# Performance work log

Measured on AMD Instinct MI355X. Metric: run time of the kernel, lower is better.

The kernel has to match this reference:

```python
import jax, jax.numpy as jnp
import numpy as np

N_HEADS = 16
DIM = 1024
HEAD_DIM = DIM // N_HEADS

def setup_inputs() -> dict:
    key = jax.random.key(0)
    ks = jax.random.split(key, 5)
    x = jax.random.normal(ks[0], (4, 2048, DIM), dtype=jnp.float32)
    W_attn = jax.random.normal(ks[1], (DIM, 3 * DIM), dtype=jnp.float32) / np.sqrt(DIM)
    b_attn = jnp.zeros((3 * DIM,), dtype=jnp.float32)
    W_proj = jax.random.normal(ks[2], (DIM, DIM), dtype=jnp.float32) / np.sqrt(DIM)
    b_proj = jnp.zeros((DIM,), dtype=jnp.float32)
    return {"x": x, "W_attn": W_attn, "b_attn": b_attn, "W_proj": W_proj, "b_proj": b_proj}

def reference(x, W_attn, b_attn, W_proj, b_proj):
    B, S, D = x.shape
    qkv = x @ W_attn + b_attn                      # [B,S,3D]
    q, k, v = jnp.split(qkv, 3, axis=2)
    def heads(t):
        return t.reshape(B, S, N_HEADS, HEAD_DIM).transpose(0, 2, 1, 3)  # [B,H,S,hd]
    qh, kh, vh = heads(q), heads(k), heads(v)
    scale = 1.0 / np.sqrt(HEAD_DIM).astype(np.float32)
    scores = jnp.einsum('bhqd,bhkd->bhqk', qh, kh) * scale  # [B,H,S,S]
    causal = jnp.tril(jnp.ones((S, S), dtype=bool))
    scores = jnp.where(causal, scores, -jnp.inf)
    probs = jax.nn.softmax(scores, axis=-1)
    ctx = jnp.einsum('bhqk,bhkd->bhqd', probs, vh)           # [B,H,S,hd]
    ctx = ctx.transpose(0, 2, 1, 3).reshape(B, S, D)
    return ctx @ W_proj + b_proj
```

## Files before the change

kernel.cpp:

```cpp
#include <hip/hip_runtime.h>
#include <hip/hip_bf16.h>
#include <stdint.h>

typedef __attribute__((ext_vector_type(4))) float  f32x4a;
typedef __attribute__((ext_vector_type(8))) short  bf16x8s;
typedef __attribute__((ext_vector_type(8))) unsigned short u16x8;

#define QSCALE 0.18033688011112042f

static __device__ __forceinline__ unsigned short f2bf(float f) {
    union { float f; uint32_t u; } v; v.f = f;
    uint32_t u = v.u;
    return (unsigned short)((u + 0x7FFFu + ((u >> 16) & 1u)) >> 16);
}

static __device__ __forceinline__ unsigned int pack2bf(float lo, float hi) {
    __hip_bfloat162 t = __float22bfloat162_rn(make_float2(lo, hi));
    union { __hip_bfloat162 b; unsigned int u; } c; c.b = t;
    return c.u;
}

static __device__ __forceinline__ float exp2a(float x) {
    float r;
    asm("v_exp_f32 %0, %1" : "=v"(r) : "v"(x));
    return r;
}

#define GLL(src, dst)                                                          \
    __builtin_amdgcn_global_load_lds(                                          \
        (const __attribute__((address_space(1))) void*)(src),                  \
        (__attribute__((address_space(3))) void*)(dst), 16, 0, 0)

__global__ __launch_bounds__(256) void k_cvt_bf16(const float* __restrict__ in,
                                                  unsigned short* __restrict__ out, int n8) {
    int i = blockIdx.x * blockDim.x + threadIdx.x;
    if (i >= n8) return;
    const float4* p = (const float4*)(in + (size_t)i * 8);
    float4 a = p[0], b = p[1];
    u16x8 o;
    o[0] = f2bf(a.x); o[1] = f2bf(a.y); o[2] = f2bf(a.z); o[3] = f2bf(a.w);
    o[4] = f2bf(b.x); o[5] = f2bf(b.y); o[6] = f2bf(b.z); o[7] = f2bf(b.w);
    *(u16x8*)(out + (size_t)i * 8) = o;
}

__global__ __launch_bounds__(256) void k_scale_bias(const float* __restrict__ b,
                                                    float* __restrict__ out,
                                                    int n, int nscale, float sc) {
    int i = blockIdx.x * blockDim.x + threadIdx.x;
    if (i >= n) return;
    out[i] = b[i] * (i < nscale ? sc : 1.0f);
}

__global__ __launch_bounds__(256) void k_transpose_w(const float* __restrict__ W,
                                                     unsigned short* __restrict__ Wt,
                                                     int K, int N, float sc, int nscale) {
    __shared__ float tile[64][68];
    int bx = blockIdx.x;
    int ntn = N >> 6;
    int kt = bx / ntn, nt = bx % ntn;
    int t = threadIdx.x;
    int r0 = t >> 4;
    int c4 = (t & 15) << 2;
    for (int i = 0; i < 4; ++i) {
        int k = r0 + i * 16;
        float4 v = *(const float4*)(W + (size_t)(kt * 64 + k) * N + nt * 64 + c4);
        tile[k][c4 + 0] = v.x; tile[k][c4 + 1] = v.y;
        tile[k][c4 + 2] = v.z; tile[k][c4 + 3] = v.w;
    }
    __syncthreads();
    int nl = t >> 2;
    int kc = (t & 3) << 4;
    float s = (nt * 64 + nl < nscale) ? sc : 1.0f;
    unsigned short* dst = Wt + (size_t)(nt * 64 + nl) * K + kt * 64 + kc;
    u16x8 o0, o1;
    for (int i = 0; i < 8; ++i) o0[i] = f2bf(tile[kc + i][nl] * s);
    for (int i = 0; i < 8; ++i) o1[i] = f2bf(tile[kc + 8 + i][nl] * s);
    *(u16x8*)dst = o0;
    *(u16x8*)(dst + 8) = o1;
}

template<int OUT_BF16, int VW>
__global__ __launch_bounds__(512, 4) void k_gemm2b(const unsigned short* __restrict__ A,
                                                   const unsigned short* __restrict__ Bt,
                                                   const float* __restrict__ bias,
                                                   void* __restrict__ Cout,
                                                   unsigned short* __restrict__ vt,
                                                   int M, int N, int K, int ntn) {
    __shared__ __align__(16) unsigned short S[3][12288];
    unsigned short* Sf = &S[0][0];

    int nwg = gridDim.x;
    int bid = blockIdx.x;
    int wg = (bid & 7) * (nwg >> 3) + (bid >> 3);
    int mt = wg / ntn, nt = wg % ntn;
    size_t m0 = (size_t)mt * 128, n0 = (size_t)nt * 256;

    int tid = threadIdx.x;
    int w = tid >> 6, lane = tid & 63;
    int wm = w >> 2, wn = w & 3;
    int l15 = lane & 15, l4 = lane >> 4;

    int srow = tid >> 2;
    int sch = (tid & 3) ^ ((srow >> 1) & 3);
    const unsigned short* Asrc = A  + (m0 + srow) * (size_t)K + sch * 8;
    const unsigned short* Bsrc = Bt + (n0 + srow) * (size_t)K + sch * 8;

#define STG(bufoff, kt)                                                                   \
    do {                                                                                  \
        GLL(Asrc + (size_t)(kt) * 32,                    Sf + (bufoff) + tid * 8);        \
        GLL(Bsrc + (size_t)(kt) * 32,                    Sf + (bufoff) + 4096 + tid * 8); \
        GLL(Bsrc + (size_t)(kt) * 32 + (size_t)128 * K,  Sf + (bufoff) + 8192 + tid * 8); \
    } while (0)

    int ck = (l4 ^ ((l15 >> 1) & 3)) * 8;
    int aoff = (wm * 64 + l15) * 32 + ck;
    int boff = 4096 + (wn * 64 + l15) * 32 + ck;

    f32x4a acc[4][4] = {};

#define BAR() __builtin_amdgcn_s_barrier()

    int NT = K >> 5;

    STG(0, 0);
    STG(12288, 1);
    asm volatile("s_waitcnt vmcnt(3)" ::: "memory");
    __builtin_amdgcn_sched_barrier(0);
    BAR();

    int cb = 0;
    for (int t = 0; t < NT; ++t) {
        int sb = cb + 24576; if (sb >= 36864) sb -= 36864;
        bool more = (t + 2) < NT;
        if (more) STG(sb, t + 2);
        bf16x8s af[4], bf[4];
        #pragma unroll
        for (int q = 0; q < 4; ++q) af[q] = *(const bf16x8s*)(Sf + cb + aoff + q * 512);
        #pragma unroll
        for (int q = 0; q < 4; ++q) bf[q] = *(const bf16x8s*)(Sf + cb + boff + q * 512);
        __builtin_amdgcn_s_setprio(1);
        #pragma unroll
        for (int mf = 0; mf < 4; ++mf)
            #pragma unroll
            for (int nf = 0; nf < 4; ++nf)
                acc[mf][nf] = __builtin_amdgcn_mfma_f32_16x16x32_bf16(af[mf], bf[nf],
                                                                      acc[mf][nf], 0, 0, 0);
        __builtin_amdgcn_s_setprio(0);
        if (more) { asm volatile("s_waitcnt vmcnt(3)" ::: "memory"); }
        else      { asm volatile("s_waitcnt vmcnt(0)" ::: "memory"); }
        __builtin_amdgcn_sched_barrier(0);
        BAR();
        cb += 12288; if (cb >= 36864) cb = 0;
    }

    if (VW && nt >= 8) {
        int b = (int)(m0 >> 11);
        int sb_ = ((int)m0 & 2047) + wm * 64;
        #pragma unroll
        for (int nf = 0; nf < 4; ++nf) {
            int vc = ((int)n0 - 2048) + wn * 64 + nf * 16 + l15;
            int h = vc >> 6, d = vc & 63;
            float bv = bias[2048 + vc];
            unsigned short* vrow = vt + ((size_t)(b * 16 + h) * 64 + d) * 2048;
            #pragma unroll
            for (int mf = 0; mf < 4; ++mf) {
                int s = sb_ + mf * 16 + l4 * 4;
                uint2 pv = make_uint2(pack2bf(acc[mf][nf][0] + bv, acc[mf][nf][1] + bv),
                                      pack2bf(acc[mf][nf][2] + bv, acc[mf][nf][3] + bv));
                *(uint2*)(vrow + s) = pv;
            }
        }
    } else {
        #pragma unroll
        for (int nf = 0; nf < 4; ++nf) {
            int col = (int)n0 + wn * 64 + nf * 16 + l15;
            float bv = bias[col];
            #pragma unroll
            for (int mf = 0; mf < 4; ++mf) {
                int rbase = (int)m0 + wm * 64 + mf * 16 + l4 * 4;
                #pragma unroll
                for (int rr = 0; rr < 4; ++rr) {
                    float v = acc[mf][nf][rr] + bv;
                    if (OUT_BF16)
                        ((unsigned short*)Cout)[(size_t)(rbase + rr) * N + col] = f2bf(v);
                    else
                        ((float*)Cout)[(size_t)(rbase + rr) * N + col] = v;
                }
            }
        }
    }
#undef STG
#undef BAR
}

__global__ __launch_bounds__(256, 4) void k_attn(const unsigned short* __restrict__ qkv,
                                                 const unsigned short* __restrict__ vt,
                                                 unsigned short* __restrict__ ctx) {
    __shared__ unsigned short Ks[2][4096];
    __shared__ unsigned short Vs[2][4096];
    __shared__ unsigned short Pb[4][1024];
    int bx = blockIdx.x;
    int bh = bx & 63;
    int pr = bx >> 6;
    int b = bh >> 4, hd = bh & 15;
    int tid = threadIdx.x;
    int w = tid >> 6, lane = tid & 63;
    int l15 = lane & 15, l4 = lane >> 4;

    const unsigned short* Qb  = qkv + (size_t)b * 2048 * 3072 + hd * 64;
    const unsigned short* Kb  = Qb + 1024;
    const unsigned short* Vtb = vt + (size_t)bh * 64 * 2048;

    int kr0 = tid >> 3, kc0 = tid & 7;
    int kr1 = (tid + 256) >> 3, kc1 = tid & 7;
    const unsigned short* Ksr0 = Kb  + (size_t)kr0 * 3072 + ((kc0 ^ (kr0 & 7)) << 3);
    const unsigned short* Ksr1 = Kb  + (size_t)kr1 * 3072 + ((kc1 ^ (kr1 & 7)) << 3);
    const unsigned short* Vsr0 = Vtb + (size_t)kr0 * 2048 + ((kc0 ^ (kr0 & 7)) << 3);
    const unsigned short* Vsr1 = Vtb + (size_t)kr1 * 2048 + ((kc1 ^ (kr1 & 7)) << 3);
    unsigned short* pbw = &Pb[w][0];

    int prow = l15 * 64;
    int psw  = l15 & 7;
    int ph   = (l4 & 1) * 4;
    int pc0  = ((0 + (l4 >> 1)) ^ psw) * 8;
    int pc1  = ((2 + (l4 >> 1)) ^ psw) * 8;
    int pc2  = ((4 + (l4 >> 1)) ^ psw) * 8;
    int pc3  = ((6 + (l4 >> 1)) ^ psw) * 8;
    int pr0  = ((0 + l4) ^ psw) * 8;
    int pr1  = ((4 + l4) ^ psw) * 8;

#define STAGE(buf, kv0s)                                                                        \
    do {                                                                                        \
        size_t ko_ = (size_t)(kv0s) * 3072;                                                     \
        GLL(Ksr0 + ko_,     &Ks[buf][w * 512]);                                                 \
        GLL(Ksr1 + ko_,     &Ks[buf][2048 + w * 512]);                                          \
        GLL(Vsr0 + (kv0s),  &Vs[buf][w * 512]);                                                 \
        GLL(Vsr1 + (kv0s),  &Vs[buf][2048 + w * 512]);                                          \
    } while (0)

    for (int half = 0; half < 2; ++half) {
        int j = half ? (31 - pr) : pr;
        int q0 = j * 64 + w * 16;
        int qa = q0 + l15;
        bf16x8s qf0, qf1;
        {
            const unsigned short* p = Qb + (size_t)(q0 + l15) * 3072 + l4 * 8;
            qf0 = *(const bf16x8s*)p;
            qf1 = *(const bf16x8s*)(p + 32);
        }
        f32x4a o[4] = {};
        float lrow = 0.0f;
        const int NSTEPS = j + 1;

        STAGE(0, 0);
        __syncthreads();

        int s = 0;
        while (true) {
            int cur = s & 1;
            int kv0 = s << 6;
            if (s + 1 < NSTEPS) STAGE(cur ^ 1, kv0 + 64);

            const unsigned short* Kbuf = Ks[cur];
            const unsigned short* Vbuf = Vs[cur];

            f32x4a z[4];
            __builtin_amdgcn_s_setprio(1);
            #pragma unroll
            for (int f = 0; f < 4; ++f) {
                int rk = f * 16 + l15;
                bf16x8s ka = *(const bf16x8s*)(Kbuf + rk * 64 + ((l4 ^ psw) << 3));
                bf16x8s kb = *(const bf16x8s*)(Kbuf + rk * 64 + (((4 + l4) ^ psw) << 3));
                f32x4a zz = {0.f, 0.f, 0.f, 0.f};
                zz = __builtin_amdgcn_mfma_f32_16x16x32_bf16(ka, qf0, zz, 0, 0, 0);
                zz = __builtin_amdgcn_mfma_f32_16x16x32_bf16(kb, qf1, zz, 0, 0, 0);
                z[f] = zz;
            }
            __builtin_amdgcn_s_setprio(0);

            bf16x8s vf[2][4];
            #pragma unroll
            for (int g = 0; g < 2; ++g)
                #pragma unroll
                for (int nf = 0; nf < 4; ++nf) {
                    int rv = nf * 16 + l15;
                    vf[g][nf] = *(const bf16x8s*)(Vbuf + rv * 64 + (((g * 4 + l4) ^ (rv & 7)) << 3));
                }

            if (s == NSTEPS - 1) {
                #pragma unroll
                for (int f = 0; f < 4; ++f)
                    #pragma unroll
                    for (int r = 0; r < 4; ++r)
                        if (kv0 + f * 16 + l4 * 4 + r > qa) z[f][r] = -1e30f;
            }

            f32x4a p4[4];
            #pragma unroll
            for (int f = 0; f < 4; ++f)
                #pragma unroll
                for (int r = 0; r < 4; ++r)
                    p4[f][r] = exp2a(z[f][r]);

            f32x4a ps = (p4[0] + p4[1]) + (p4[2] + p4[3]);
            float psum = (ps[0] + ps[1]) + (ps[2] + ps[3]);
            psum += __shfl_xor(psum, 16);
            psum += __shfl_xor(psum, 32);
            lrow += psum;

            unsigned int pk[8];
            #pragma unroll
            for (int f = 0; f < 4; ++f) {
                pk[2 * f]     = pack2bf(p4[f][0], p4[f][1]);
                pk[2 * f + 1] = pack2bf(p4[f][2], p4[f][3]);
            }

            *(uint2*)(pbw + prow + pc0 + ph) = make_uint2(pk[0], pk[1]);
            *(uint2*)(pbw + prow + pc1 + ph) = make_uint2(pk[2], pk[3]);
            *(uint2*)(pbw + prow + pc2 + ph) = make_uint2(pk[4], pk[5]);
            *(uint2*)(pbw + prow + pc3 + ph) = make_uint2(pk[6], pk[7]);
            asm volatile("" ::: "memory");
            bf16x8s pa0 = *(const bf16x8s*)(pbw + prow + pr0);
            bf16x8s pa1 = *(const bf16x8s*)(pbw + prow + pr1);
            asm volatile("" ::: "memory");

            __builtin_amdgcn_s_setprio(1);
            #pragma unroll
            for (int nf = 0; nf < 4; ++nf)
                o[nf] = __builtin_amdgcn_mfma_f32_16x16x32_bf16(pa0, vf[0][nf], o[nf], 0, 0, 0);
            #pragma unroll
            for (int nf = 0; nf < 4; ++nf)
                o[nf] = __builtin_amdgcn_mfma_f32_16x16x32_bf16(pa1, vf[1][nf], o[nf], 0, 0, 0);
            __builtin_amdgcn_s_setprio(0);

            ++s;
            if (s == NSTEPS) break;
            __syncthreads();
        }
        __syncthreads();

        float linv[4];
        #pragma unroll
        for (int r = 0; r < 4; ++r) linv[r] = 1.0f / __shfl(lrow, l4 * 4 + r);
        #pragma unroll
        for (int nf = 0; nf < 4; ++nf) {
            int col = hd * 64 + nf * 16 + l15;
            #pragma unroll
            for (int r = 0; r < 4; ++r) {
                int row = q0 + l4 * 4 + r;
                ctx[((size_t)b * 2048 + row) * 1024 + col] = f2bf(o[nf][r] * linv[r]);
            }
        }
    }
#undef STAGE
}

extern "C" void kernel_launch(void* const* d_in, const int* in_sizes, int n_in,
                              void* d_out, int out_size, void* d_ws, size_t ws_size,
                              hipStream_t stream) {
    const float* x      = (const float*)d_in[0];
    const float* W_attn = (const float*)d_in[1];
    const float* b_attn = (const float*)d_in[2];
    const float* W_proj = (const float*)d_in[3];
    const float* b_proj = (const float*)d_in[4];

    char* ws = (char*)d_ws;
    unsigned short* xb  = (unsigned short*)ws; ws += (size_t)8192 * 1024 * 2;
    unsigned short* wta = (unsigned short*)ws; ws += (size_t)3072 * 1024 * 2;
    unsigned short* wtp = (unsigned short*)ws; ws += (size_t)1024 * 1024 * 2;
    unsigned short* qkv = (unsigned short*)ws; ws += (size_t)8192 * 3072 * 2;
    unsigned short* vt  = (unsigned short*)ws; ws += (size_t)64 * 64 * 2048 * 2;
    unsigned short* ctx = (unsigned short*)ws; ws += (size_t)8192 * 1024 * 2;
    float*          sbias = (float*)ws;

    k_cvt_bf16<<<4096, 256, 0, stream>>>(x, xb, 8192 * 1024 / 8);
    k_transpose_w<<<16 * 48, 256, 0, stream>>>(W_attn, wta, 1024, 3072, QSCALE, 1024);
    k_transpose_w<<<16 * 16, 256, 0, stream>>>(W_proj, wtp, 1024, 1024, 1.0f, 0);
    k_scale_bias<<<12, 256, 0, stream>>>(b_attn, sbias, 3072, 1024, QSCALE);
    k_gemm2b<1, 1><<<768, 512, 0, stream>>>(xb, wta, sbias, (void*)qkv, vt, 8192, 3072, 1024, 12);
    k_attn<<<1024, 256, 0, stream>>>(qkv, vt, ctx);
    k_gemm2b<0, 0><<<256, 512, 0, stream>>>(ctx, wtp, b_proj, d_out, nullptr, 8192, 1024, 1024, 4);
}
```

Baseline: 161.9 us.

## Enlarge attention query tile to 128 rows so each K/V tile serves two query groups

Result: no change. 160.8 us (-0.6%).

```diff
diff --git a/kernel.cpp b/kernel.cpp
--- a/kernel.cpp
+++ b/kernel.cpp
@@ -193,12 +193,12 @@
 #undef BAR
 }
 
-__global__ __launch_bounds__(256, 4) void k_attn(const unsigned short* __restrict__ qkv,
+__global__ __launch_bounds__(256, 2) void k_attn(const unsigned short* __restrict__ qkv,
                                                  const unsigned short* __restrict__ vt,
                                                  unsigned short* __restrict__ ctx) {
     __shared__ unsigned short Ks[2][4096];
     __shared__ unsigned short Vs[2][4096];
-    __shared__ unsigned short Pb[4][1024];
+    __shared__ unsigned short Pb[4][2048];
     int bx = blockIdx.x;
     int bh = bx & 63;
     int pr = bx >> 6;
@@ -219,7 +219,6 @@
     const unsigned short* Vsr1 = Vtb + (size_t)kr1 * 2048 + ((kc1 ^ (kr1 & 7)) << 3);
     unsigned short* pbw = &Pb[w][0];
 
-    int prow = l15 * 64;
     int psw  = l15 & 7;
     int ph   = (l4 & 1) * 4;
     int pc0  = ((0 + (l4 >> 1)) ^ psw) * 8;
@@ -228,6 +227,8 @@
     int pc3  = ((6 + (l4 >> 1)) ^ psw) * 8;
     int pr0  = ((0 + l4) ^ psw) * 8;
     int pr1  = ((4 + l4) ^ psw) * 8;
+    int prow0 = l15 * 64;
+    int prow1 = (l15 + 16) * 64;
 
 #define STAGE(buf, kv0s)                                                                        \
     do {                                                                                        \
@@ -239,18 +240,21 @@
     } while (0)
 
     for (int half = 0; half < 2; ++half) {
-        int j = half ? (31 - pr) : pr;
-        int q0 = j * 64 + w * 16;
-        int qa = q0 + l15;
-        bf16x8s qf0, qf1;
+        int j = half ? (15 - pr) : pr;
+        int q0 = j * 128 + w * 32;
+        int qa0 = q0 + l15, qa1 = q0 + 16 + l15;
+        bf16x8s qf[2][2];
         {
-            const unsigned short* p = Qb + (size_t)(q0 + l15) * 3072 + l4 * 8;
-            qf0 = *(const bf16x8s*)p;
-            qf1 = *(const bf16x8s*)(p + 32);
-        }
-        f32x4a o[4] = {};
-        float lrow = 0.0f;
-        const int NSTEPS = j + 1;
+            const unsigned short* p0 = Qb + (size_t)(q0 + l15) * 3072 + l4 * 8;
+            qf[0][0] = *(const bf16x8s*)p0;
+            qf[0][1] = *(const bf16x8s*)(p0 + 32);
+            const unsigned short* p1 = p0 + (size_t)16 * 3072;
+            qf[1][0] = *(const bf16x8s*)p1;
+            qf[1][1] = *(const bf16x8s*)(p1 + 32);
+        }
+        f32x4a o[2][4] = {};
+        float lrow0 = 0.0f, lrow1 = 0.0f;
+        const int NSTEPS = 2 * j + 2;
 
         STAGE(0, 0);
         __syncthreads();
@@ -261,77 +265,103 @@
             int kv0 = s << 6;
             if (s + 1 < NSTEPS) STAGE(cur ^ 1, kv0 + 64);
 
-            const unsigned short* Kbuf = Ks[cur];
-            const unsigned short* Vbuf = Vs[cur];
-
-            f32x4a z[4];
-            __builtin_amdgcn_s_setprio(1);
-            #pragma unroll
-            for (int f = 0; f < 4; ++f) {
-                int rk = f * 16 + l15;
-                bf16x8s ka = *(const bf16x8s*)(Kbuf + rk * 64 + ((l4 ^ psw) << 3));
-                bf16x8s kb = *(const bf16x8s*)(Kbuf + rk * 64 + (((4 + l4) ^ psw) << 3));
-                f32x4a zz = {0.f, 0.f, 0.f, 0.f};
-                zz = __builtin_amdgcn_mfma_f32_16x16x32_bf16(ka, qf0, zz, 0, 0, 0);
-                zz = __builtin_amdgcn_mfma_f32_16x16x32_bf16(kb, qf1, zz, 0, 0, 0);
-                z[f] = zz;
+            if (kv0 <= q0 + 31) {
+                const unsigned short* Kbuf = Ks[cur];
+                const unsigned short* Vbuf = Vs[cur];
+
+                f32x4a z[2][4];
+                __builtin_amdgcn_s_setprio(1);
+                #pragma unroll
+                for (int f = 0; f < 4; ++f) {
+                    int rk = f * 16 + l15;
+                    bf16x8s ka = *(const bf16x8s*)(Kbuf + rk * 64 + ((l4 ^ psw) << 3));
+                    bf16x8s kb = *(const bf16x8s*)(Kbuf + rk * 64 + (((4 + l4) ^ psw) << 3));
+                    #pragma unroll
+                    for (int g = 0; g < 2; ++g) {
+                        f32x4a zz = {0.f, 0.f, 0.f, 0.f};
+                        zz = __builtin_amdgcn_mfma_f32_16x16x32_bf16(ka, qf[g][0], zz, 0, 0, 0);
+                        zz = __builtin_amdgcn_mfma_f32_16x16x32_bf16(kb, qf[g][1], zz, 0, 0, 0);
+                        z[g][f] = zz;
+                    }
+                }
+                __builtin_amdgcn_s_setprio(0);
+
+                bf16x8s vf[2][4];
+                #pragma unroll
+                for (int g = 0; g < 2; ++g)
+                    #pragma unroll
+                    for (int nf = 0; nf < 4; ++nf) {
+                        int rv = nf * 16 + l15;
+                        vf[g][nf] = *(const bf16x8s*)(Vbuf + rv * 64 + (((g * 4 + l4) ^ (rv & 7)) << 3));
+                    }
+
+                if (kv0 + 63 > q0) {
+                    #pragma unroll
+                    for (int f = 0; f < 4; ++f)
+                        #pragma unroll
+                        for (int r = 0; r < 4; ++r) {
+                            int kvp = kv0 + f * 16 + l4 * 4 + r;
+                            if (kvp > qa0) z[0][f][r] = -1e30f;
+                            if (kvp > qa1) z[1][f][r] = -1e30f;
+                        }
+                }
+
+                f32x4a p4[2][4];
+                #pragma unroll
+                for (int g = 0; g < 2; ++g)
+                    #pragma unroll
+                    for (int f = 0; f < 4; ++f)
+                        #pragma unroll
+                        for (int r = 0; r < 4; ++r)
+                            p4[g][f][r] = exp2a(z[g][f][r]);
+
+                f32x4a ps0 = (p4[0][0] + p4[0][1]) + (p4[0][2] + p4[0][3]);
+                f32x4a ps1 = (p4[1][0] + p4[1][1]) + (p4[1][2] + p4[1][3]);
+                float psum0 = (ps0[0] + ps0[1]) + (ps0[2] + ps0[3]);
+                float psum1 = (ps1[0] + ps1[1]) + (ps1[2] + ps1[3]);
+                psum0 += __shfl_xor(psum0, 16);
+                psum0 += __shfl_xor(psum0, 32);
+                psum1 += __shfl_xor(psum1, 16);
+                psum1 += __shfl_xor(psum1, 32);
+                lrow0 += psum0;
+                lrow1 += psum1;
+
+                unsigned int pk[2][8];
+                #pragma unroll
+                for (int g = 0; g < 2; ++g)
+                    #pragma unroll
+                    for (int f = 0; f < 4; ++f) {
+                        pk[g][2 * f]     = pack2bf(p4[g][f][0], p4[g][f][1]);
+                        pk[g][2 * f + 1] = pack2bf(p4[g][f][2], p4[g][f][3]);
+                    }
+
+                *(uint2*)(pbw + prow0 + pc0 + ph) = make_uint2(pk[0][0], pk[0][1]);
+                *(uint2*)(pbw + prow0 + pc1 + ph) = make_uint2(pk[0][2], pk[0][3]);
+                *(uint2*)(pbw + prow0 + pc2 + ph) = make_uint2(pk[0][4], pk[0][5]);
+                *(uint2*)(pbw + prow0 + pc3 + ph) = make_uint2(pk[0][6], pk[0][7]);
+                *(uint2*)(pbw + prow1 + pc0 + ph) = make_uint2(pk[1][0], pk[1][1]);
+                *(uint2*)(pbw + prow1 + pc1 + ph) = make_uint2(pk[1][2], pk[1][3]);
+                *(uint2*)(pbw + prow1 + pc2 + ph) = make_uint2(pk[1][4], pk[1][5]);
+                *(uint2*)(pbw + prow1 + pc3 + ph) = make_uint2(pk[1][6], pk[1][7]);
+                asm volatile("" ::: "memory");
+                bf16x8s pa[2][2];
+                pa[0][0] = *(const bf16x8s*)(pbw + prow0 + pr0);
+                pa[0][1] = *(const bf16x8s*)(pbw + prow0 + pr1);
+                pa[1][0] = *(const bf16x8s*)(pbw + prow1 + pr0);
+                pa[1][1] = *(const bf16x8s*)(pbw + prow1 + pr1);
+                asm volatile("" ::: "memory");
+
+                __builtin_amdgcn_s_setprio(1);
+                #pragma unroll
+                for (int hh = 0; hh < 2; ++hh)
+                    #pragma unroll
+                    for (int g = 0; g < 2; ++g)
+                        #pragma unroll
+                        for (int nf = 0; nf < 4; ++nf)
+                            o[g][nf] = __builtin_amdgcn_mfma_f32_16x16x32_bf16(
+                                pa[g][hh], vf[hh][nf], o[g][nf], 0, 0, 0);
+                __builtin_amdgcn_s_setprio(0);
             }
-            __builtin_amdgcn_s_setprio(0);
-
-            bf16x8s vf[2][4];
-            #pragma unroll
-            for (int g = 0; g < 2; ++g)
-                #pragma unroll
-                for (int nf = 0; nf < 4; ++nf) {
-                    int rv = nf * 16 + l15;
-                    vf[g][nf] = *(const bf16x8s*)(Vbuf + rv * 64 + (((g * 4 + l4) ^ (rv & 7)) << 3));
-                }
-
-            if (s == NSTEPS - 1) {
-                #pragma unroll
-                for (int f = 0; f < 4; ++f)
-                    #pragma unroll
-                    for (int r = 0; r < 4; ++r)
-                        if (kv0 + f * 16 + l4 * 4 + r > qa) z[f][r] = -1e30f;
-            }
-
-            f32x4a p4[4];
-            #pragma unroll
-            for (int f = 0; f < 4; ++f)
-                #pragma unroll
-                for (int r = 0; r < 4; ++r)
-                    p4[f][r] = exp2a(z[f][r]);
-
-            f32x4a ps = (p4[0] + p4[1]) + (p4[2] + p4[3]);
-            float psum = (ps[0] + ps[1]) + (ps[2] + ps[3]);
-            psum += __shfl_xor(psum, 16);
-            psum += __shfl_xor(psum, 32);
-            lrow += psum;
-
-            unsigned int pk[8];
-            #pragma unroll
-            for (int f = 0; f < 4; ++f) {
-                pk[2 * f]     = pack2bf(p4[f][0], p4[f][1]);
-                pk[2 * f + 1] = pack2bf(p4[f][2], p4[f][3]);
-            }
-
-            *(uint2*)(pbw + prow + pc0 + ph) = make_uint2(pk[0], pk[1]);
-            *(uint2*)(pbw + prow + pc1 + ph) = make_uint2(pk[2], pk[3]);
-            *(uint2*)(pbw + prow + pc2 + ph) = make_uint2(pk[4], pk[5]);
-            *(uint2*)(pbw + prow + pc3 + ph) = make_uint2(pk[6], pk[7]);
-            asm volatile("" ::: "memory");
-            bf16x8s pa0 = *(const bf16x8s*)(pbw + prow + pr0);
-            bf16x8s pa1 = *(const bf16x8s*)(pbw + prow + pr1);
-            asm volatile("" ::: "memory");
-
-            __builtin_amdgcn_s_setprio(1);
-            #pragma unroll
-            for (int nf = 0; nf < 4; ++nf)
-                o[nf] = __builtin_amdgcn_mfma_f32_16x16x32_bf16(pa0, vf[0][nf], o[nf], 0, 0, 0);
-            #pragma unroll
-            for (int nf = 0; nf < 4; ++nf)
-                o[nf] = __builtin_amdgcn_mfma_f32_16x16x32_bf16(pa1, vf[1][nf], o[nf], 0, 0, 0);
-            __builtin_amdgcn_s_setprio(0);
 
             ++s;
             if (s == NSTEPS) break;
@@ -339,16 +369,20 @@
         }
         __syncthreads();
 
-        float linv[4];
-        #pragma unroll
-        for (int r = 0; r < 4; ++r) linv[r] = 1.0f / __shfl(lrow, l4 * 4 + r);
+        float linv0[4], linv1[4];
+        #pragma unroll
+        for (int r = 0; r < 4; ++r) {
+            linv0[r] = 1.0f / __shfl(lrow0, l4 * 4 + r);
+            linv1[r] = 1.0f / __shfl(lrow1, l4 * 4 + r);
+        }
         #pragma unroll
         for (int nf = 0; nf < 4; ++nf) {
             int col = hd * 64 + nf * 16 + l15;
             #pragma unroll
             for (int r = 0; r < 4; ++r) {
-                int row = q0 + l4 * 4 + r;
-                ctx[((size_t)b * 2048 + row) * 1024 + col] = f2bf(o[nf][r] * linv[r]);
+                int row0 = q0 + l4 * 4 + r;
+                ctx[((size_t)b * 2048 + row0) * 1024 + col]      = f2bf(o[0][nf][r] * linv0[r]);
+                ctx[((size_t)b * 2048 + row0 + 16) * 1024 + col] = f2bf(o[1][nf][r] * linv1[r]);
             }
         }
     }
@@ -378,6 +412,6 @@
     k_transpose_w<<<16 * 16, 256, 0, stream>>>(W_proj, wtp, 1024, 1024, 1.0f, 0);
     k_scale_bias<<<12, 256, 0, stream>>>(b_attn, sbias, 3072, 1024, QSCALE);
     k_gemm2b<1, 1><<<768, 512, 0, stream>>>(xb, wta, sbias, (void*)qkv, vt, 8192, 3072, 1024, 12);
-    k_attn<<<1024, 256, 0, stream>>>(qkv, vt, ctx);
+    k_attn<<<512, 256, 0, stream>>>(qkv, vt, ctx);
     k_gemm2b<0, 0><<<256, 512, 0, stream>>>(ctx, wtp, b_proj, d_out, nullptr, 8192, 1024, 1024, 4);
 }
```
